# Kernel tuning notes

Measured on AMD Instinct MI355X. Metric: run time of the kernel, lower is better.

## Reference

```python
import jax, jax.numpy as jnp
import numpy as np

# --- static anchor geometry (exactly mirrors RPN._make_anchor_box) ---

def _valid_idx():
    scales = [64.0, 128.0, 256.0]
    ratios = [0.5, 1.0, 2.0]
    # (h, w) per anchor, normalized by 448
    anc = np.array([[s / np.sqrt(r), s * np.sqrt(r)] for s in scales for r in ratios]) / 448.0
    c = (np.arange(28) + 0.5) / 28.0
    cy = np.repeat(c, 28).reshape(28, 28)  # y varies along rows
    cx = np.tile(c, (28, 1))               # x varies along cols
    boxes = np.zeros((28, 28, 36))
    for a in range(9):
        boxes[..., 4 * a + 0] = cy
        boxes[..., 4 * a + 1] = cx
        boxes[..., 4 * a + 2] = anc[a, 0]
        boxes[..., 4 * a + 3] = anc[a, 1]
    b = boxes.reshape(-1, 4)  # [7056, 4] in yxhw
    y1 = b[:, 0] - b[:, 2] / 2
    x1 = b[:, 1] - b[:, 3] / 2
    y2 = b[:, 0] + b[:, 2] / 2
    x2 = b[:, 1] + b[:, 3] / 2
    return np.where((y1 > 0) & (x1 > 0) & (y2 < 28) & (x2 < 28))[0]

_VALID = _valid_idx()  # 4850 static indices

ROI_CLS_THRESHOLD = 0.9


def setup_inputs() -> dict:
    key = jax.random.key(0)
    ks = jax.random.split(key, 4)
    C = 2048
    return {
        'x': jax.random.normal(ks[0], (1, C, 28, 28), jnp.float32),
        'conv_w': jax.random.normal(ks[1], (C, C, 3, 3), jnp.float32) * 0.02,
        'conv_b': jnp.zeros((C,), jnp.float32),
        'reg_w': jax.random.normal(ks[2], (36, C), jnp.float32) * 0.02,
        'reg_b': jnp.zeros((36,), jnp.float32),
        'cls_w': jax.random.normal(ks[3], (9, C), jnp.float32) * 0.02,
        'cls_b': jnp.zeros((9,), jnp.float32),
    }


def reference(x, conv_w, conv_b, reg_w, reg_b, cls_w, cls_b):
    # Conv block: 3x3 conv + BatchNorm(identity at init: gamma=1, beta=0, running stats 0/1) + ReLU
    h = jax.lax.conv_general_dilated(
        x, conv_w, window_strides=(1, 1), padding=((1, 1), (1, 1)),
        dimension_numbers=('NCHW', 'OIHW', 'NCHW'))
    h = jax.nn.relu(h + conv_b[None, :, None, None])
    # 1x1 conv heads + sigmoid
    reg = jax.nn.sigmoid(jnp.einsum('bchw,oc->bohw', h, reg_w) + reg_b[None, :, None, None])  # [1,36,28,28]
    cls = jax.nn.sigmoid(jnp.einsum('bchw,oc->bohw', h, cls_w) + cls_b[None, :, None, None])  # [1,9,28,28]
    # exact replication of view/permute/squeeze + static valid-anchor gather
    reg = reg.reshape(1, 4, -1).transpose(0, 2, 1)[0][_VALID]  # [4850, 4]
    cls = cls.reshape(-1)[_VALID]                              # [4850]
    # inference path (gt=None): reg[cls > 0.9]; fixed-shape masked equivalent
    keep = cls > ROI_CLS_THRESHOLD
    return reg * keep[:, None]
```

## Files before the change

kernel.cpp:

```cpp
#include <hip/hip_runtime.h>
#include <cstdint>

typedef __attribute__((ext_vector_type(8))) short s8v;
typedef __attribute__((ext_vector_type(4))) float f4v;

__device__ __forceinline__ unsigned short bf16_rne(float f) {
    unsigned u = __float_as_uint(f);
    u += 0x7FFFu + ((u >> 16) & 1u);
    return (unsigned short)(u >> 16);
}
__device__ __forceinline__ float bf16f(unsigned short h) {
    return __uint_as_float(((unsigned)h) << 16);
}
__device__ __forceinline__ void cvt2(float a, float b, unsigned& hiw, unsigned& low) {
    unsigned ua = __float_as_uint(a), ub = __float_as_uint(b);
    unsigned ha = ua + 0x7FFFu + ((ua >> 16) & 1u);
    unsigned hb = ub + 0x7FFFu + ((ub >> 16) & 1u);
    hiw = (ha >> 16) | (hb & 0xFFFF0000u);
    float ra = a - __uint_as_float(ha & 0xFFFF0000u);
    float rb = b - __uint_as_float(hb & 0xFFFF0000u);
    unsigned la = __float_as_uint(ra), lb = __float_as_uint(rb);
    la += 0x7FFFu + ((la >> 16) & 1u);
    lb += 0x7FFFu + ((lb >> 16) & 1u);
    low = (la >> 16) | (lb & 0xFFFF0000u);
}
__device__ __forceinline__ void cvt2t(float a, float b, unsigned& hiw, unsigned& low) {
    unsigned ua = __float_as_uint(a), ub = __float_as_uint(b);
    hiw = (ua >> 16) | (ub & 0xFFFF0000u);
    float ra = a - __uint_as_float(ua & 0xFFFF0000u);
    float rb = b - __uint_as_float(ub & 0xFFFF0000u);
    unsigned la = __float_as_uint(ra), lb = __float_as_uint(rb);
    low = (la >> 16) | (lb & 0xFFFF0000u);
}

__global__ __launch_bounds__(256) void transpose_x(const float* __restrict__ x,
                                                   float* __restrict__ xt) {
    __shared__ float t[64][65];
    int c0 = blockIdx.x * 64, p0 = blockIdx.y * 64;
    int l = threadIdx.x & 63, g = threadIdx.x >> 6;
#pragma unroll
    for (int j = 0; j < 16; ++j) {
        int cc = j * 4 + g;
        int p = p0 + l;
        t[cc][l] = (p < 784) ? x[(size_t)(c0 + cc) * 784 + p] : 0.f;
    }
    __syncthreads();
#pragma unroll
    for (int j = 0; j < 16; ++j) {
        int pp = j * 4 + g;
        int p = p0 + pp;
        if (p < 784) xt[(size_t)p * 2048 + c0 + l] = t[l][pp];
    }
}

__global__ __launch_bounds__(256) void build_B(const float* __restrict__ xt,
                                               unsigned* __restrict__ Bhi,
                                               unsigned* __restrict__ Blo) {
    int p = blockIdx.x;
    int h = p / 28, w = p % 28;
#pragma unroll
    for (int it = 0; it < 4; ++it) {
        int cp = it * 256 + threadIdx.x;
        float va[18];
#pragma unroll
        for (int r = 0; r < 9; ++r) {
            int h2 = h + r / 3 - 1, w2 = w + r % 3 - 1;
            bool ok = (h2 >= 0) & (h2 < 28) & (w2 >= 0) & (w2 < 28);
            float2 v = ok ? ((const float2*)(xt + (size_t)(h2 * 28 + w2) * 2048))[cp]
                          : float2{0.f, 0.f};
            va[r] = v.x;
            va[9 + r] = v.y;
        }
        size_t base = (size_t)p * 9216 + (size_t)cp * 9;
#pragma unroll
        for (int d = 0; d < 9; ++d) {
            unsigned hw, lw;
            cvt2(va[2 * d], va[2 * d + 1], hw, lw);
            Bhi[base + d] = hw;
            Blo[base + d] = lw;
        }
    }
}

#define KCH 1152
#define NSTEP 36
#define LDS_BYTES 61440

__global__ __launch_bounds__(256, 2) void conv_gemm(const float* __restrict__ cw,
                                                    const char* __restrict__ wsb,
                                                    uint32_t offBhi, uint32_t offBlo,
                                                    float* __restrict__ part) {
    __shared__ char smem[LDS_BYTES];
    int tid = threadIdx.x;
    int lane = tid & 63, wave = tid >> 6;
    int bm0 = blockIdx.x * 128, bn0 = blockIdx.y * 112, z = blockIdx.z;

    uint32_t doff[4], dldsB[4];
#pragma unroll
    for (int j = 0; j < 4; ++j) {
        int i = j * 4 + wave;
        if (i >= 14) i -= 2;
        bool hiP = i < 7;
        int jj = hiP ? i : i - 7;
        int prow = jj * 16 + (lane >> 2);
        int pos = lane & 3;
        int gblk = pos ^ ((prow >> 1) & 3);
        uint32_t elem = (uint32_t)(bn0 + prow) * 18432 + (uint32_t)z * KCH + gblk * 8;
        doff[j] = (hiP ? offBhi : offBlo) + elem * 2;
        dldsB[j] = (hiP ? 0u : 7168u) + (uint32_t)jj * 1024;
    }

    int m = lane & 15, qd = lane >> 4;
    int sw = (m >> 1) & 3;
    uint32_t apos = (uint32_t)(wave * 32 + m) * 64 + (uint32_t)((qd ^ sw) * 16);
    uint32_t bpos = (uint32_t)m * 64 + (uint32_t)((qd ^ sw) * 16);
    int arow = tid >> 1, ahalf = tid & 1;
    int swt = (arow >> 1) & 3;

    f4v acc[2][7];
#pragma unroll
    for (int a = 0; a < 2; ++a)
#pragma unroll
        for (int b = 0; b < 7; ++b) acc[a][b] = f4v{0.f, 0.f, 0.f, 0.f};

    const float4* ap = (const float4*)(cw + (size_t)(bm0 + arow) * 18432 + (size_t)z * KCH
                                       + (size_t)ahalf * 16);
    float4 ar[4];
#pragma unroll
    for (int j = 0; j < 4; ++j) ar[j] = ap[j];

    auto writeA = [&](char* smA) {
        unsigned hw[8], lw[8];
#pragma unroll
        for (int j = 0; j < 4; ++j) {
            cvt2t(ar[j].x, ar[j].y, hw[2 * j], lw[2 * j]);
            cvt2t(ar[j].z, ar[j].w, hw[2 * j + 1], lw[2 * j + 1]);
        }
#pragma unroll
        for (int b = 0; b < 2; ++b) {
            uint32_t col = (uint32_t)(((2 * ahalf + b) ^ swt) * 16);
            *(uint4*)(smA + arow * 64 + col) =
                uint4{hw[4 * b], hw[4 * b + 1], hw[4 * b + 2], hw[4 * b + 3]};
            *(uint4*)(smA + 8192 + arow * 64 + col) =
                uint4{lw[4 * b], lw[4 * b + 1], lw[4 * b + 2], lw[4 * b + 3]};
        }
    };

#pragma unroll
    for (int j = 0; j < 4; ++j) {
        __builtin_amdgcn_global_load_lds(
            (const __attribute__((address_space(1))) void*)(wsb + doff[j]),
            (__attribute__((address_space(3))) void*)(smem + 32768 + dldsB[j]), 16, 0, 0);
        doff[j] += 64;
    }
    writeA(smem);
    ap += 8;
#pragma unroll
    for (int j = 0; j < 4; ++j) ar[j] = ap[j];
    __syncthreads();

#pragma unroll 2
    for (int step = 0; step < NSTEP; ++step) {
        int buf = step & 1, nbuf = buf ^ 1;
        char* smA = smem + buf * 16384;
        char* smB = smem + 32768 + buf * 14336;

        if (step < NSTEP - 1) {
            char* smBn = smem + 32768 + nbuf * 14336;
#pragma unroll
            for (int j = 0; j < 4; ++j) {
                __builtin_amdgcn_global_load_lds(
                    (const __attribute__((address_space(1))) void*)(wsb + doff[j]),
                    (__attribute__((address_space(3))) void*)(smBn + dldsB[j]), 16, 0, 0);
                doff[j] += 64;
            }
            writeA(smem + nbuf * 16384);
            if (step < NSTEP - 2) {
                ap += 8;
#pragma unroll
                for (int j = 0; j < 4; ++j) ar[j] = ap[j];
            }
        }

        s8v ah[2], al[2];
#pragma unroll
        for (int mt = 0; mt < 2; ++mt) {
            ah[mt] = *(const s8v*)(smA + apos + mt * 1024);
            al[mt] = *(const s8v*)(smA + 8192 + apos + mt * 1024);
        }
        __builtin_amdgcn_s_setprio(1);
#pragma unroll
        for (int nt = 0; nt < 7; ++nt) {
            s8v bh = *(const s8v*)(smB + bpos + nt * 1024);
            s8v bl = *(const s8v*)(smB + 7168 + bpos + nt * 1024);
#pragma unroll
            for (int mt = 0; mt < 2; ++mt) {
                acc[mt][nt] = __builtin_amdgcn_mfma_f32_16x16x32_bf16(ah[mt], bh, acc[mt][nt], 0, 0, 0);
                acc[mt][nt] = __builtin_amdgcn_mfma_f32_16x16x32_bf16(ah[mt], bl, acc[mt][nt], 0, 0, 0);
                acc[mt][nt] = __builtin_amdgcn_mfma_f32_16x16x32_bf16(al[mt], bh, acc[mt][nt], 0, 0, 0);
            }
        }
        __builtin_amdgcn_s_setprio(0);
        __syncthreads();
    }

    float* pz = part + (size_t)z * 1605632;
#pragma unroll
    for (int mt = 0; mt < 2; ++mt) {
        int o = bm0 + wave * 32 + mt * 16 + qd * 4;
#pragma unroll
        for (int nt = 0; nt < 7; ++nt) {
            int p = bn0 + nt * 16 + m;
            *(float4*)(pz + (size_t)p * 2048 + o) =
                float4{acc[mt][nt].x, acc[mt][nt].y, acc[mt][nt].z, acc[mt][nt].w};
        }
    }
}

__constant__ int HMIN_d[9] = {3, 2, 1, 6, 4, 3, 11, 8, 6};
__constant__ int WMIN_d[9] = {1, 2, 3, 3, 4, 6, 6, 8, 11};

__global__ __launch_bounds__(256) void heads(const float* __restrict__ part,
                                             const float* __restrict__ conv_b,
                                             const float* __restrict__ reg_w,
                                             const float* __restrict__ reg_b,
                                             const float* __restrict__ cls_w,
                                             const float* __restrict__ cls_b,
                                             float* __restrict__ out) {
    int tid = threadIdx.x;
    int lane = tid & 63, wave = tid >> 6;
    int p = blockIdx.x;
    int ci = tid * 2;

    float4 h0 = ((const float4*)conv_b)[ci];
    float4 h1 = ((const float4*)conv_b)[ci + 1];
#pragma unroll
    for (int z = 0; z < 16; ++z) {
        const float4* pz = (const float4*)(part + (size_t)z * 1605632 + (size_t)p * 2048);
        float4 a = pz[ci], b = pz[ci + 1];
        h0.x += a.x; h0.y += a.y; h0.z += a.z; h0.w += a.w;
        h1.x += b.x; h1.y += b.y; h1.z += b.z; h1.w += b.w;
    }
    h0.x = fmaxf(h0.x, 0.f); h0.y = fmaxf(h0.y, 0.f);
    h0.z = fmaxf(h0.z, 0.f); h0.w = fmaxf(h0.w, 0.f);
    h1.x = fmaxf(h1.x, 0.f); h1.y = fmaxf(h1.y, 0.f);
    h1.z = fmaxf(h1.z, 0.f); h1.w = fmaxf(h1.w, 0.f);

    float s[45];
#pragma unroll
    for (int o = 0; o < 36; ++o) {
        float4 wa = ((const float4*)(reg_w + (size_t)o * 2048))[ci];
        float4 wb = ((const float4*)(reg_w + (size_t)o * 2048))[ci + 1];
        s[o] = h0.x * wa.x + h0.y * wa.y + h0.z * wa.z + h0.w * wa.w +
               h1.x * wb.x + h1.y * wb.y + h1.z * wb.z + h1.w * wb.w;
    }
#pragma unroll
    for (int a = 0; a < 9; ++a) {
        float4 wa = ((const float4*)(cls_w + (size_t)a * 2048))[ci];
        float4 wb = ((const float4*)(cls_w + (size_t)a * 2048))[ci + 1];
        s[36 + a] = h0.x * wa.x + h0.y * wa.y + h0.z * wa.z + h0.w * wa.w +
                    h1.x * wb.x + h1.y * wb.y + h1.z * wb.z + h1.w * wb.w;
    }

    __shared__ float wsum[4][45];
    __shared__ float fin[45];
#pragma unroll
    for (int o = 0; o < 45; ++o) {
        float v = s[o];
#pragma unroll
        for (int d = 1; d < 64; d <<= 1) v += __shfl_xor(v, d, 64);
        if (lane == 0) wsum[wave][o] = v;
    }
    __syncthreads();
    if (tid < 45) fin[tid] = wsum[0][tid] + wsum[1][tid] + wsum[2][tid] + wsum[3][tid];
    __syncthreads();

    if (tid < 9) {
        int ap = tid;
        int n = ap * 784 + p;
        int pix = n / 9, a2 = n % 9;
        int hh = pix / 28, ww = pix % 28;
        if (hh >= HMIN_d[a2] && ww >= WMIN_d[a2]) {
            int row = 0;
#pragma unroll
            for (int a3 = 0; a3 < 9; ++a3) {
                int hm = HMIN_d[a3], wm = WMIN_d[a3];
                int full = hh - hm; if (full < 0) full = 0;
                row += full * (28 - wm);
                if (hh >= hm) { int prt = ww - wm; if (prt < 0) prt = 0; row += prt; }
                if (a3 < a2 && hh >= hm && ww >= wm) row += 1;
            }
            float cl = fin[36 + ap] + cls_b[ap];
            float keep = (1.f / (1.f + expf(-cl)) > 0.9f) ? 1.f : 0.f;
#pragma unroll
            for (int q = 0; q < 4; ++q) {
                float rl = fin[q * 9 + ap] + reg_b[q * 9 + ap];
                out[row * 4 + q] = keep / (1.f + expf(-rl));
            }
        }
    }
}

extern "C" void kernel_launch(void* const* d_in, const int* in_sizes, int n_in,
                              void* d_out, int out_size, void* d_ws, size_t ws_size,
                              hipStream_t stream) {
    const float* x = (const float*)d_in[0];
    const float* conv_w = (const float*)d_in[1];
    const float* conv_b = (const float*)d_in[2];
    const float* reg_w = (const float*)d_in[3];
    const float* reg_b = (const float*)d_in[4];
    const float* cls_w = (const float*)d_in[5];
    const float* cls_b = (const float*)d_in[6];
    float* out = (float*)d_out;
    char* ws = (char*)d_ws;

    const size_t o_part = 0;
    const size_t o_xt = 0;
    const size_t o_Bhi = 102760448;
    const size_t o_Blo = 131661824;

    transpose_x<<<dim3(32, 13), 256, 0, stream>>>(x, (float*)(ws + o_xt));
    build_B<<<784, 256, 0, stream>>>((const float*)(ws + o_xt), (unsigned*)(ws + o_Bhi),
                                     (unsigned*)(ws + o_Blo));
    conv_gemm<<<dim3(16, 7, 16), 256, 0, stream>>>(conv_w, ws, (uint32_t)o_Bhi,
                                                   (uint32_t)o_Blo, (float*)(ws + o_part));
    heads<<<784, 256, 0, stream>>>((const float*)(ws + o_part), conv_b, reg_w, reg_b,
                                   cls_w, cls_b, out);
}
```

Measured before the change: 524.0 us.

## Load A operand directly into MFMA registers, dropping LDS staging for A

```diff
diff --git a/kernel.cpp b/kernel.cpp
--- a/kernel.cpp
+++ b/kernel.cpp
@@ -32,6 +32,16 @@
     unsigned la = __float_as_uint(ra), lb = __float_as_uint(rb);
     low = (la >> 16) | (lb & 0xFFFF0000u);
 }
+__device__ __forceinline__ void cvt8(float4 a, float4 b, s8v& hi, s8v& lo) {
+    unsigned h0, h1, h2, h3, l0, l1, l2, l3;
+    cvt2t(a.x, a.y, h0, l0);
+    cvt2t(a.z, a.w, h1, l1);
+    cvt2t(b.x, b.y, h2, l2);
+    cvt2t(b.z, b.w, h3, l3);
+    uint4 uh{h0, h1, h2, h3}, ul{l0, l1, l2, l3};
+    hi = *(s8v*)&uh;
+    lo = *(s8v*)&ul;
+}
 
 __global__ __launch_bounds__(256) void transpose_x(const float* __restrict__ x,
                                                    float* __restrict__ xt) {
@@ -84,9 +94,9 @@
 
 #define KCH 1152
 #define NSTEP 36
-#define LDS_BYTES 61440
-
-__global__ __launch_bounds__(256, 2) void conv_gemm(const float* __restrict__ cw,
+#define LDS_BYTES 28672
+
+__global__ __launch_bounds__(256, 4) void conv_gemm(const float* __restrict__ cw,
                                                     const char* __restrict__ wsb,
                                                     uint32_t offBhi, uint32_t offBlo,
                                                     float* __restrict__ part) {
@@ -112,61 +122,42 @@
 
     int m = lane & 15, qd = lane >> 4;
     int sw = (m >> 1) & 3;
-    uint32_t apos = (uint32_t)(wave * 32 + m) * 64 + (uint32_t)((qd ^ sw) * 16);
     uint32_t bpos = (uint32_t)m * 64 + (uint32_t)((qd ^ sw) * 16);
-    int arow = tid >> 1, ahalf = tid & 1;
-    int swt = (arow >> 1) & 3;
+
+    const float4* ap0 = (const float4*)(cw + (size_t)(bm0 + wave * 32 + m) * 18432
+                                        + (size_t)z * KCH + (size_t)qd * 8);
+    const float4* ap1 = (const float4*)(cw + (size_t)(bm0 + wave * 32 + 16 + m) * 18432
+                                        + (size_t)z * KCH + (size_t)qd * 8);
 
     f4v acc[2][7];
 #pragma unroll
     for (int a = 0; a < 2; ++a)
 #pragma unroll
         for (int b = 0; b < 7; ++b) acc[a][b] = f4v{0.f, 0.f, 0.f, 0.f};
-
-    const float4* ap = (const float4*)(cw + (size_t)(bm0 + arow) * 18432 + (size_t)z * KCH
-                                       + (size_t)ahalf * 16);
-    float4 ar[4];
-#pragma unroll
-    for (int j = 0; j < 4; ++j) ar[j] = ap[j];
-
-    auto writeA = [&](char* smA) {
-        unsigned hw[8], lw[8];
-#pragma unroll
-        for (int j = 0; j < 4; ++j) {
-            cvt2t(ar[j].x, ar[j].y, hw[2 * j], lw[2 * j]);
-            cvt2t(ar[j].z, ar[j].w, hw[2 * j + 1], lw[2 * j + 1]);
-        }
-#pragma unroll
-        for (int b = 0; b < 2; ++b) {
-            uint32_t col = (uint32_t)(((2 * ahalf + b) ^ swt) * 16);
-            *(uint4*)(smA + arow * 64 + col) =
-                uint4{hw[4 * b], hw[4 * b + 1], hw[4 * b + 2], hw[4 * b + 3]};
-            *(uint4*)(smA + 8192 + arow * 64 + col) =
-                uint4{lw[4 * b], lw[4 * b + 1], lw[4 * b + 2], lw[4 * b + 3]};
-        }
-    };
 
 #pragma unroll
     for (int j = 0; j < 4; ++j) {
         __builtin_amdgcn_global_load_lds(
             (const __attribute__((address_space(1))) void*)(wsb + doff[j]),
-            (__attribute__((address_space(3))) void*)(smem + 32768 + dldsB[j]), 16, 0, 0);
+            (__attribute__((address_space(3))) void*)(smem + dldsB[j]), 16, 0, 0);
         doff[j] += 64;
     }
-    writeA(smem);
-    ap += 8;
-#pragma unroll
-    for (int j = 0; j < 4; ++j) ar[j] = ap[j];
+    s8v ah[2], al[2], ahn[2], aln[2];
+    {
+        float4 a0 = ap0[0], a1 = ap0[1], a2 = ap1[0], a3 = ap1[1];
+        ap0 += 8;
+        ap1 += 8;
+        cvt8(a0, a1, ah[0], al[0]);
+        cvt8(a2, a3, ah[1], al[1]);
+    }
     __syncthreads();
 
 #pragma unroll 2
     for (int step = 0; step < NSTEP; ++step) {
-        int buf = step & 1, nbuf = buf ^ 1;
-        char* smA = smem + buf * 16384;
-        char* smB = smem + 32768 + buf * 14336;
-
+        char* smB = smem + (step & 1) * 14336;
+        float4 a0, a1, a2, a3;
         if (step < NSTEP - 1) {
-            char* smBn = smem + 32768 + nbuf * 14336;
+            char* smBn = smem + ((step & 1) ^ 1) * 14336;
 #pragma unroll
             for (int j = 0; j < 4; ++j) {
                 __builtin_amdgcn_global_load_lds(
@@ -174,20 +165,14 @@
                     (__attribute__((address_space(3))) void*)(smBn + dldsB[j]), 16, 0, 0);
                 doff[j] += 64;
             }
-            writeA(smem + nbuf * 16384);
-            if (step < NSTEP - 2) {
-                ap += 8;
-#pragma unroll
-                for (int j = 0; j < 4; ++j) ar[j] = ap[j];
-            }
-        }
-
-        s8v ah[2], al[2];
-#pragma unroll
-        for (int mt = 0; mt < 2; ++mt) {
-            ah[mt] = *(const s8v*)(smA + apos + mt * 1024);
-            al[mt] = *(const s8v*)(smA + 8192 + apos + mt * 1024);
-        }
+            a0 = ap0[0];
+            a1 = ap0[1];
+            a2 = ap1[0];
+            a3 = ap1[1];
+            ap0 += 8;
+            ap1 += 8;
+        }
+
         __builtin_amdgcn_s_setprio(1);
 #pragma unroll
         for (int nt = 0; nt < 7; ++nt) {
@@ -201,7 +186,16 @@
             }
         }
         __builtin_amdgcn_s_setprio(0);
+
+        if (step < NSTEP - 1) {
+            cvt8(a0, a1, ahn[0], aln[0]);
+            cvt8(a2, a3, ahn[1], aln[1]);
+        }
         __syncthreads();
+        ah[0] = ahn[0];
+        ah[1] = ahn[1];
+        al[0] = aln[0];
+        al[1] = aln[1];
     }
 
     float* pz = part + (size_t)z * 1605632;
```

After: 505.3 us. 3.6% less time.
